# Optimization experiments

Hardware: AMD Instinct MI355X
Metric: run time of the kernel (lower is better)

Reference implementation:

```python
import jax, jax.numpy as jnp
import numpy as np

MAX_ITER = 10   # float32 branch of cg()
TOL = 1e-10

def _cdot(a, b):
    # complex_dot: sum(conj(a) * b) over all elements
    return jnp.sum(jnp.conj(a) * b)

def _A(p, smaps, mask):
    # p: [H,W] complex, smaps: [C,H,W] complex, mask: [H,W] real
    return jnp.fft.fft2(smaps * p[None], norm='ortho') * mask[None]

def _AH(y, smaps, mask):
    imgs = jnp.fft.ifft2(y * mask[None], norm='ortho')
    return jnp.sum(jnp.conj(smaps) * imgs, axis=0)  # [H,W]

def _cg(M, rhs):
    # conjugate gradient, faithful to the TF while_loop body
    def cond(s):
        i, rTr, x, r, p = s
        return jnp.logical_and(i < MAX_ITER, rTr > TOL)
    def body(s):
        i, rTr, x, r, p = s
        Ap = M(p)
        alpha = rTr / jnp.real(_cdot(p, Ap))
        x = x + p * alpha
        r = r - Ap * alpha
        rTrNew = jnp.real(_cdot(r, r))
        beta = rTrNew / rTr
        p = r + p * beta
        return (i + 1, rTrNew, x, r, p)
    rTr0 = jnp.real(_cdot(rhs, rhs))
    s0 = (jnp.int32(0), rTr0, jnp.zeros_like(rhs), rhs, rhs)
    return jax.lax.while_loop(cond, body, s0)[2]

def _solve_one(lambdaa, rhs, smaps, mask):
    M = lambda p: _AH(_A(p, smaps, mask), smaps, mask) + p * lambdaa
    return _cg(M, rhs)

_solve_b = jax.vmap(_solve_one, in_axes=(None, 0, 0, 0))  # replaces map_fn
_AH_b = jax.vmap(_AH, in_axes=(0, 0, 0))

def setup_inputs():
    key = jax.random.key(0)
    ks = jax.random.split(key, 7)
    B, C, H, W = 4, 16, 384, 384
    f = lambda k, s: jax.random.normal(k, s, dtype=jnp.float32)
    return {
        'lambdaa': 0.05 * jnp.ones((), jnp.float32),
        'x_re': f(ks[0], (B, H, W)),
        'x_im': f(ks[1], (B, H, W)),
        'y_re': f(ks[2], (B, C, H, W)),
        'y_im': f(ks[3], (B, C, H, W)),
        'smaps_re': f(ks[4], (B, C, H, W)),
        'smaps_im': f(ks[5], (B, C, H, W)),
        'mask': (jax.random.uniform(ks[6], (B, H, W)) < 0.33).astype(jnp.float32),
    }

def reference(lambdaa, x_re, x_im, y_re, y_im, smaps_re, smaps_im, mask):
    x = jax.lax.complex(x_re, x_im)
    y = jax.lax.complex(y_re, y_im)
    smaps = jax.lax.complex(smaps_re, smaps_im)
    # rhs = AH(y) + lambdaa * x
    rhs = _AH_b(y, smaps, mask) + x * lambdaa
    out = _solve_b(lambdaa, rhs, smaps, mask)  # [B,H,W] complex
    return jnp.stack([out.real, out.imag], axis=-1)  # [B,H,W,2] float32
```

## Files before the change

### kernel.cpp

```cpp
#include <hip/hip_runtime.h>
#include <hip/hip_fp16.h>


#define Bn 4
#define Cn 16
#define Hn 384
#define Wn 384
#define NPIX (Hn*Wn)
#define NPIX2 (NPIX/2)
#define TPB 256
#define CTPB 512
#define NCOL 16
#define TOLF 1e-10f
#define NITER 10
#define RED_BLKS 72
#define GRP 4
#define CPG 4
#define RPITCH 416
#define CPITCH 417

__device__ __forceinline__ float2 cadd(float2 a, float2 b){ return make_float2(a.x+b.x, a.y+b.y); }
__device__ __forceinline__ float2 csub(float2 a, float2 b){ return make_float2(a.x-b.x, a.y-b.y); }
__device__ __forceinline__ float2 cmulf(float2 a, float2 b){
  return make_float2(a.x*b.x - a.y*b.y, a.x*b.y + a.y*b.x);
}

__device__ __forceinline__ void wave_fence(){ asm volatile("s_waitcnt lgkmcnt(0)" ::: "memory"); }

template<int IMM>
__device__ __forceinline__ float2 shx(float2 v){
  int x = __builtin_amdgcn_ds_swizzle(__float_as_int(v.x), IMM);
  int y = __builtin_amdgcn_ds_swizzle(__float_as_int(v.y), IMM);
  return make_float2(__int_as_float(x), __int_as_float(y));
}

__device__ __forceinline__ int rev5(int x){
  return ((x&1)<<4) | ((x&2)<<2) | (x&4) | ((x&8)>>2) | ((x&16)>>4);
}

__device__ __forceinline__ int offmap(int w){ return w + ((w*683)>>13); }

template<int DIR>
__device__ __forceinline__ void fft12(float2* v)
{
  const float S3 = (DIR<0) ? -0.86602540378443864676f : 0.86602540378443864676f;
  const float sg = (DIR<0) ? -1.f : 1.f;
  float2 t[4][3];
#pragma unroll
  for (int b = 0; b < 4; ++b) {
    float2 a0 = v[b], a1 = v[4+b], a2 = v[8+b];
    float2 s = cadd(a1,a2), d = csub(a1,a2);
    float2 mm = make_float2(a0.x - 0.5f*s.x, a0.y - 0.5f*s.y);
    float2 e  = make_float2(-d.y*S3, d.x*S3);
    t[b][0] = cadd(a0,s);
    t[b][1] = cadd(mm,e);
    t[b][2] = csub(mm,e);
  }
  const float2 w1  = make_float2(0.86602540378443864676f, sg*0.5f);
  const float2 w2  = make_float2(0.5f, sg*0.86602540378443864676f);
  const float2 w3  = make_float2(0.f, sg);
  const float2 w4t = make_float2(-0.5f, sg*0.86602540378443864676f);
  const float2 w6  = make_float2(-1.f, 0.f);
  t[1][1] = cmulf(t[1][1], w1);  t[1][2] = cmulf(t[1][2], w2);
  t[2][1] = cmulf(t[2][1], w2);  t[2][2] = cmulf(t[2][2], w4t);
  t[3][1] = cmulf(t[3][1], w3);  t[3][2] = cmulf(t[3][2], w6);
#pragma unroll
  for (int c = 0; c < 3; ++c) {
    float2 e = cadd(t[0][c], t[2][c]);
    float2 f = csub(t[0][c], t[2][c]);
    float2 g = cadd(t[1][c], t[3][c]);
    float2 h = csub(t[1][c], t[3][c]);
    float2 ih = (DIR<0) ? make_float2(h.y, -h.x) : make_float2(-h.y, h.x);
    v[c]   = cadd(e,g);
    v[c+3] = cadd(f,ih);
    v[c+6] = csub(e,g);
    v[c+9] = csub(f,ih);
  }
}

template<int DIR>
__device__ __forceinline__ void fft32_lanes(float2* v, int li)
{
  const float c2pi = (DIR<0) ? -6.2831853071795864769f : 6.2831853071795864769f;
  const float sg   = (DIR<0) ? -1.f : 1.f;
  float s, c;
  __sincosf(c2pi*(1.f/32.f)*(float)(li&15), &s, &c); float2 wA = make_float2(c,s);
  __sincosf(c2pi*(1.f/16.f)*(float)(li&7),  &s, &c); float2 wB = make_float2(c,s);
  __sincosf(c2pi*(1.f/ 8.f)*(float)(li&3),  &s, &c); float2 wC = make_float2(c,s);
  bool bA = li & 16, bB = li & 8, bC = li & 4, bD = li & 2, bE = li & 1;
#pragma unroll
  for (int k = 0; k < 12; ++k) {
    float2 a = v[k], o;
    o = shx<0x401F>(a); a = bA ? cmulf(csub(o,a), wA) : cadd(a,o);
    o = shx<0x201F>(a); a = bB ? cmulf(csub(o,a), wB) : cadd(a,o);
    o = shx<0x101F>(a); a = bC ? cmulf(csub(o,a), wC) : cadd(a,o);
    o = shx<0x081F>(a);
    { float2 su = cadd(a,o), d = csub(o,a);
      float2 dw = bE ? make_float2(-sg*d.y, sg*d.x) : d;
      a = bD ? dw : su; }
    o = shx<0x041F>(a); a = bE ? csub(o,a) : cadd(a,o);
    v[k] = a;
  }
}

template<int DIR>
__device__ __forceinline__ void fft32_lanes_dit(float2* v, int li)
{
  const float c2pi = (DIR<0) ? -6.2831853071795864769f : 6.2831853071795864769f;
  const float sg   = (DIR<0) ? -1.f : 1.f;
  float s, c;
  __sincosf(c2pi*(1.f/32.f)*(float)(li&15), &s, &c); float2 wA = make_float2(c,s);
  __sincosf(c2pi*(1.f/16.f)*(float)(li&7),  &s, &c); float2 wB = make_float2(c,s);
  __sincosf(c2pi*(1.f/ 8.f)*(float)(li&3),  &s, &c); float2 wC = make_float2(c,s);
  bool bA = li & 16, bB = li & 8, bC = li & 4, bD = li & 2, bE = li & 1;
#pragma unroll
  for (int k = 0; k < 12; ++k) {
    float2 a = v[k], o;
    o = shx<0x041F>(a); a = bE ? csub(o,a) : cadd(a,o);
    { float2 aw = make_float2(-sg*a.y, sg*a.x);
      a = (bD && bE) ? aw : a;
      o = shx<0x081F>(a); a = bD ? csub(o,a) : cadd(a,o); }
    { float2 aw = cmulf(a, wC); a = bC ? aw : a;
      o = shx<0x101F>(a); a = bC ? csub(o,a) : cadd(a,o); }
    { float2 aw = cmulf(a, wB); a = bB ? aw : a;
      o = shx<0x201F>(a); a = bB ? csub(o,a) : cadd(a,o); }
    { float2 aw = cmulf(a, wA); a = bA ? aw : a;
      o = shx<0x401F>(a); a = bA ? csub(o,a) : cadd(a,o); }
    v[k] = a;
  }
}

template<int DIR>
__device__ __forceinline__ void fft384(float2* v, int li)
{
  fft12<DIR>(v);
  const float c2pi = (DIR<0) ? -6.2831853071795864769f : 6.2831853071795864769f;
  float s, c;
  __sincosf(c2pi*(1.f/384.f)*(float)li, &s, &c);
  float2 W = make_float2(c,s), cw = W;
#pragma unroll
  for (int k = 1; k < 12; ++k) { v[k] = cmulf(v[k], cw); cw = cmulf(cw, W); }
  fft32_lanes<DIR>(v, li);
}

template<int DIR>
__device__ __forceinline__ void fft384_scr(float2* v, int li)
{
  fft32_lanes_dit<DIR>(v, li);
  const float c2pi = (DIR<0) ? -6.2831853071795864769f : 6.2831853071795864769f;
  float s, c;
  __sincosf(c2pi*(1.f/384.f)*(float)li, &s, &c);
  float2 W = make_float2(c,s), cw = W;
#pragma unroll
  for (int k = 1; k < 12; ++k) { v[k] = cmulf(v[k], cw); cw = cmulf(cw, W); }
  fft12<DIR>(v);
}


template<bool HS>
__global__ __launch_bounds__(TPB) void k_row_fwd(
    const float2* __restrict__ p, const float* __restrict__ Sre,
    const float* __restrict__ Sim, const __half2* __restrict__ Sh,
    __half2* __restrict__ tmp)
{
  int tid = threadIdx.x;
  int wave = tid>>6, lane = tid&63, sub = lane>>5, li = lane&31;
  int row = wave*2 + sub;
  int tile = blockIdx.x % (Hn/8);
  int bc   = blockIdx.x / (Hn/8);
  int b = bc / Cn;
  int h = tile*8 + row;
  size_t gbase = (size_t)bc*NPIX + (size_t)h*Wn;
  size_t pbase = (size_t)b*NPIX + (size_t)h*Wn;

  float2 v[12];
#pragma unroll
  for (int k = 0; k < 12; ++k) {
    int w = 32*k + li;
    float2 pv = p[pbase + w];
    float sr, si;
    if (HS) { float2 sv = __half22float2(Sh[gbase + w]); sr = sv.x; si = sv.y; }
    else    { sr = Sre[gbase + w]; si = Sim[gbase + w]; }
    v[k] = make_float2(sr*pv.x - si*pv.y, sr*pv.y + si*pv.x);
  }
  fft384<-1>(v, li);
#pragma unroll
  for (int k = 0; k < 12; ++k)
    tmp[gbase + 32*k + li] = __float22half2_rn(v[k]);
}

template<bool HS>
__global__ __launch_bounds__(TPB) void k_row_inv_scr(
    const __half2* __restrict__ tmp, const float* __restrict__ Sre,
    const float* __restrict__ Sim, const __half2* __restrict__ Sh,
    float2* __restrict__ partial)
{
  int tid = threadIdx.x;
  int wave = tid>>6, lane = tid&63, sub = lane>>5, li = lane&31;
  int row = wave*2 + sub;
  int tile = blockIdx.x % (Hn/8);
  int rest = blockIdx.x / (Hn/8);
  int g = rest % GRP;
  int b = rest / GRP;
  int h = tile*8 + row;

  size_t gbase0 = ((size_t)b*Cn + g*CPG)*NPIX + (size_t)h*Wn;
  __half2 hb[12];
#pragma unroll
  for (int k = 0; k < 12; ++k) hb[k] = tmp[gbase0 + 32*k + li];

  float2 acc[12];
#pragma unroll
  for (int k = 0; k < 12; ++k) acc[k] = make_float2(0.f, 0.f);

  for (int j = 0; j < CPG; ++j) {
    size_t gb = gbase0 + (size_t)j*NPIX;
    float2 vc[12];
#pragma unroll
    for (int k = 0; k < 12; ++k) vc[k] = __half22float2(hb[k]);
    if (j + 1 < CPG) {
      size_t gbn = gb + NPIX;
#pragma unroll
      for (int k = 0; k < 12; ++k) hb[k] = tmp[gbn + 32*k + li];
    }
    fft384_scr<1>(vc, li);
#pragma unroll
    for (int k = 0; k < 12; ++k) {
      int w = 32*k + li;
      float sr, si;
      if (HS) { float2 sv = __half22float2(Sh[gb + w]); sr = sv.x; si = sv.y; }
      else    { sr = Sre[gb + w]; si = Sim[gb + w]; }
      acc[k].x += sr*vc[k].x + si*vc[k].y;
      acc[k].y += sr*vc[k].y - si*vc[k].x;
    }
  }
  size_t pbase = ((size_t)g*Bn + b)*NPIX + (size_t)h*Wn;
#pragma unroll
  for (int k = 0; k < 12; ++k) partial[pbase + 32*k + li] = acc[k];
}

__global__ __launch_bounds__(TPB) void k_row_inv_nat(
    const __half2* __restrict__ tmp, const float* __restrict__ Sre,
    const float* __restrict__ Sim, float2* __restrict__ partial)
{
  __shared__ float2 lbuf[8*RPITCH];
  int tid = threadIdx.x;
  int wave = tid>>6, lane = tid&63, sub = lane>>5, li = lane&31;
  int row = wave*2 + sub;
  int tile = blockIdx.x % (Hn/8);
  int rest = blockIdx.x / (Hn/8);
  int g = rest % GRP;
  int b = rest / GRP;
  int h = tile*8 + row;
  int m = rev5(li);
  float2* lrow = lbuf + row*RPITCH;

  size_t gbase0 = ((size_t)b*Cn + g*CPG)*NPIX + (size_t)h*Wn;
  __half2 hb[12];
#pragma unroll
  for (int k = 0; k < 12; ++k) hb[k] = tmp[gbase0 + 32*k + li];

  float2 acc[12];
#pragma unroll
  for (int k = 0; k < 12; ++k) acc[k] = make_float2(0.f, 0.f);

  for (int j = 0; j < CPG; ++j) {
    size_t gb = gbase0 + (size_t)j*NPIX;
    float2 vc[12];
#pragma unroll
    for (int k = 0; k < 12; ++k) vc[k] = __half22float2(hb[k]);
    if (j + 1 < CPG) {
      size_t gbn = gb + NPIX;
#pragma unroll
      for (int k = 0; k < 12; ++k) hb[k] = tmp[gbn + 32*k + li];
    }
    fft384<1>(vc, li);
    wave_fence();
#pragma unroll
    for (int k = 0; k < 12; ++k) lrow[13*m + k] = vc[k];
    wave_fence();
#pragma unroll
    for (int k = 0; k < 12; ++k) {
      int w = 32*k + li;
      float2 u = lrow[offmap(w)];
      float sr = Sre[gb + w], si = Sim[gb + w];
      acc[k].x += sr*u.x + si*u.y;
      acc[k].y += sr*u.y - si*u.x;
    }
  }
  size_t pbase = ((size_t)g*Bn + b)*NPIX + (size_t)h*Wn;
#pragma unroll
  for (int k = 0; k < 12; ++k) partial[pbase + 32*k + li] = acc[k];
}

__global__ __launch_bounds__(TPB) void k_spack(
    const float* __restrict__ sre, const float* __restrict__ sim,
    __half2* __restrict__ sh)
{
  size_t i = (size_t)blockIdx.x*TPB + threadIdx.x;
  if (i < (size_t)Bn*Cn*NPIX) sh[i] = __floats2half2_rn(sre[i], sim[i]);
}

__global__ __launch_bounds__(TPB) void k_maskp(
    const float* __restrict__ mask, float* __restrict__ maskP,
    float* __restrict__ scal)
{
  int idx = blockIdx.x*TPB + threadIdx.x;
  if (blockIdx.x == 0) scal[threadIdx.x] = 0.0f;
  if (idx >= Bn*NPIX) return;
  int k = idx % 12; int t = idx / 12;
  int li = t & 31; t >>= 5;
  int wa = t % Wn; int b = t / Wn;
  int wt = (wa >> 5) + 12*rev5(wa & 31);
  maskP[idx] = mask[((size_t)b*Hn + (k + 12*rev5(li)))*Wn + wt] * (1.0f/(float)NPIX);
}

__global__ __launch_bounds__(CTPB) void k_col_full(
    __half2* __restrict__ tmp, const float* __restrict__ maskP)
{
  __shared__ __half2 dbuf[NCOL*CPITCH];
  int tid = threadIdx.x;
  int wave = tid>>6, lane = tid&63, sub = lane>>5, li = lane&31;
  int col = wave*2 + sub;
  int tile = blockIdx.x % (Wn/NCOL);
  int bc   = blockIdx.x / (Wn/NCOL);
  int b = bc / Cn;
  int w0 = tile*NCOL;
  size_t tbase = (size_t)bc*NPIX;

  for (int e = tid; e < NCOL*Hn; e += CTPB) {
    int wi = e & (NCOL-1), h = e >> 4;
    dbuf[wi*CPITCH + offmap(h)] = tmp[tbase + (size_t)h*Wn + w0 + wi];
  }
  __syncthreads();

  __half2* drow = dbuf + col*CPITCH;
  int w = w0 + col;
  const float4* mp4 = (const float4*)(maskP + (((size_t)b*Wn + w)*32 + li)*12);
  float4 m0 = mp4[0], m1 = mp4[1], m2 = mp4[2];
  float2 v[12];
#pragma unroll
  for (int k = 0; k < 12; ++k) v[k] = __half22float2(drow[offmap(32*k + li)]);
  fft384<-1>(v, li);
  float mk[12] = {m0.x,m0.y,m0.z,m0.w, m1.x,m1.y,m1.z,m1.w, m2.x,m2.y,m2.z,m2.w};
#pragma unroll
  for (int k = 0; k < 12; ++k) v[k] = make_float2(v[k].x*mk[k], v[k].y*mk[k]);
  fft384_scr<1>(v, li);
#pragma unroll
  for (int k = 0; k < 12; ++k) drow[offmap(32*k + li)] = __float22half2_rn(v[k]);
  __syncthreads();

  for (int e = tid; e < NCOL*Hn; e += CTPB) {
    int wi = e & (NCOL-1), h = e >> 4;
    tmp[tbase + (size_t)h*Wn + w0 + wi] = dbuf[wi*CPITCH + offmap(h)];
  }
}

__global__ __launch_bounds__(CTPB) void k_col_rhs(
    const float* __restrict__ yre, const float* __restrict__ yim,
    const float* __restrict__ mask, __half2* __restrict__ tmp)
{
  __shared__ float2 dbuf[NCOL*CPITCH];
  int tid = threadIdx.x;
  int wave = tid>>6, lane = tid&63, sub = lane>>5, li = lane&31;
  int col = wave*2 + sub;
  int tile = blockIdx.x % (Wn/NCOL);
  int bc   = blockIdx.x / (Wn/NCOL);
  int b = bc / Cn;
  int w0 = tile*NCOL;
  size_t tbase = (size_t)bc*NPIX;
  size_t mbase = (size_t)b*NPIX;

  for (int e = tid; e < NCOL*Hn; e += CTPB) {
    int wi = e & (NCOL-1), h = e >> 4;
    size_t gi = (size_t)h*Wn + w0 + wi;
    float mv = mask[mbase + gi] * (1.0f/384.0f);
    dbuf[wi*CPITCH + offmap(h)] = make_float2(yre[tbase+gi]*mv, yim[tbase+gi]*mv);
  }
  __syncthreads();

  float2* drow = dbuf + col*CPITCH;
  int m = rev5(li);
  float2 v[12];
#pragma unroll
  for (int k = 0; k < 12; ++k) v[k] = drow[offmap(32*k + li)];
  fft384<1>(v, li);
  wave_fence();
#pragma unroll
  for (int k = 0; k < 12; ++k) drow[13*m + k] = v[k];
  __syncthreads();

  for (int e = tid; e < NCOL*Hn; e += CTPB) {
    int wi = e & (NCOL-1), h = e >> 4;
    tmp[tbase + (size_t)h*Wn + w0 + wi] = __float22half2_rn(dbuf[wi*CPITCH + offmap(h)]);
  }
}


__device__ __forceinline__ void block_reduce_atomic(float sum, float* target)
{
  __shared__ float red[TPB];
  red[threadIdx.x] = sum; __syncthreads();
  for (int s = TPB/2; s > 0; s >>= 1) {
    if (threadIdx.x < s) red[threadIdx.x] += red[threadIdx.x + s];
    __syncthreads();
  }
  if (threadIdx.x == 0) unsafeAtomicAdd(target, red[0]);
  __syncthreads();
}

__global__ __launch_bounds__(TPB) void k_rhs_init(
    const float* __restrict__ xre, const float* __restrict__ xim,
    const float* __restrict__ lam, const float2* __restrict__ partial,
    float2* __restrict__ r, float2* __restrict__ p, float2* __restrict__ x,
    float* __restrict__ scal)
{
  int b = blockIdx.y;
  float l = lam[0];
  float sum = 0.0f;
  const float2* xr2 = (const float2*)(xre + (size_t)b*NPIX);
  const float2* xi2 = (const float2*)(xim + (size_t)b*NPIX);
  float4* r4 = (float4*)(r + (size_t)b*NPIX);
  float4* p4 = (float4*)(p + (size_t)b*NPIX);
  float4* x4 = (float4*)(x + (size_t)b*NPIX);
  for (int i = blockIdx.x*TPB + threadIdx.x; i < NPIX2; i += RED_BLKS*TPB) {
    float2 re = xr2[i], im = xi2[i];
    float4 rv = make_float4(l*re.x, l*im.x, l*re.y, l*im.y);
#pragma unroll
    for (int g = 0; g < GRP; ++g) {
      float4 pv = ((const float4*)(partial + ((size_t)g*Bn + b)*NPIX))[i];
      rv.x += pv.x; rv.y += pv.y; rv.z += pv.z; rv.w += pv.w;
    }
    r4[i] = rv; p4[i] = rv;
    x4[i] = make_float4(0.f, 0.f, 0.f, 0.f);
    sum += rv.x*rv.x + rv.y*rv.y + rv.z*rv.z + rv.w*rv.w;
  }
  block_reduce_atomic(sum, &scal[b]);
}

__global__ __launch_bounds__(TPB) void k_combine_dot3(
    const float2* __restrict__ p, const float2* __restrict__ r,
    const float* __restrict__ lam, const float2* __restrict__ partial,
    float2* __restrict__ Ap, float* __restrict__ slot)
{
  int b = blockIdx.y;
  float l = lam[0];
  float s_pAp = 0.f, s_AA = 0.f, s_rA = 0.f;
  const float4* p4 = (const float4*)(p + (size_t)b*NPIX);
  const float4* r4 = (const float4*)(r + (size_t)b*NPIX);
  float4* A4 = (float4*)(Ap + (size_t)b*NPIX);
  for (int i = blockIdx.x*TPB + threadIdx.x; i < NPIX2; i += RED_BLKS*TPB) {
    float4 pv = p4[i];
    float4 av = make_float4(l*pv.x, l*pv.y, l*pv.z, l*pv.w);
#pragma unroll
    for (int g = 0; g < GRP; ++g) {
      float4 qv = ((const float4*)(partial + ((size_t)g*Bn + b)*NPIX))[i];
      av.x += qv.x; av.y += qv.y; av.z += qv.z; av.w += qv.w;
    }
    A4[i] = av;
    float4 rv = r4[i];
    s_pAp += pv.x*av.x + pv.y*av.y + pv.z*av.z + pv.w*av.w;
    s_AA  += av.x*av.x + av.y*av.y + av.z*av.z + av.w*av.w;
    s_rA  += rv.x*av.x + rv.y*av.y + rv.z*av.z + rv.w*av.w;
  }
  block_reduce_atomic(s_pAp, &slot[b]);
  block_reduce_atomic(s_AA,  &slot[4+b]);
  block_reduce_atomic(s_rA,  &slot[8+b]);
}

__global__ void k_scal(float* __restrict__ scal, int it)
{
  int b = threadIdx.x;
  if (b >= Bn) return;
  float rtr = scal[it*4 + b];
  const float* slot = scal + 64 + it*12;
  float* ab = scal + 224 + it*12;
  bool act = rtr > TOLF;
  float alpha = act ? rtr / slot[b] : 0.f;
  float rtrn = act ? fmaxf(rtr - 2.f*alpha*slot[8+b] + alpha*alpha*slot[4+b], 0.f) : rtr;
  float beta = act ? rtrn / rtr : 0.f;
  scal[(it+1)*4 + b] = rtrn;
  ab[b] = alpha; ab[4+b] = beta; ab[8+b] = act ? 1.f : 0.f;
}

__global__ __launch_bounds__(TPB) void k_upd(
    float2* __restrict__ x, float2* __restrict__ r, float2* __restrict__ p,
    const float2* __restrict__ Ap, const float* __restrict__ ab)
{
  int b = blockIdx.y;
  if (!(ab[8+b] > 0.5f)) return;
  float alpha = ab[b], beta = ab[4+b];
  float4* x4 = (float4*)(x + (size_t)b*NPIX);
  float4* r4 = (float4*)(r + (size_t)b*NPIX);
  float4* p4 = (float4*)(p + (size_t)b*NPIX);
  const float4* A4 = (const float4*)(Ap + (size_t)b*NPIX);
  for (int i = blockIdx.x*TPB + threadIdx.x; i < NPIX2; i += RED_BLKS*TPB) {
    float4 pv = p4[i], av = A4[i], xv = x4[i], rv = r4[i];
    xv.x += alpha*pv.x; xv.y += alpha*pv.y; xv.z += alpha*pv.z; xv.w += alpha*pv.w;
    rv.x -= alpha*av.x; rv.y -= alpha*av.y; rv.z -= alpha*av.z; rv.w -= alpha*av.w;
    x4[i] = xv; r4[i] = rv;
    p4[i] = make_float4(rv.x + beta*pv.x, rv.y + beta*pv.y,
                        rv.z + beta*pv.z, rv.w + beta*pv.w);
  }
}


extern "C" void kernel_launch(void* const* d_in, const int* in_sizes, int n_in,
                              void* d_out, int out_size, void* d_ws, size_t ws_size,
                              hipStream_t stream)
{
  const float* lam  = (const float*)d_in[0];
  const float* xre  = (const float*)d_in[1];
  const float* xim  = (const float*)d_in[2];
  const float* yre  = (const float*)d_in[3];
  const float* yim  = (const float*)d_in[4];
  const float* sre  = (const float*)d_in[5];
  const float* sim  = (const float*)d_in[6];
  const float* mask = (const float*)d_in[7];

  const size_t szTmp  = (size_t)Bn*Cn*NPIX*sizeof(__half2);
  const size_t szVec  = (size_t)Bn*NPIX*sizeof(float2);
  const size_t szMask = (size_t)Bn*NPIX*sizeof(float);
  const size_t szSh   = (size_t)Bn*Cn*NPIX*sizeof(__half2);
  const size_t base   = szTmp + (size_t)GRP*szVec + 3*szVec + 2048 + szMask;
  const bool useSh    = (ws_size >= base + szSh);

  char* ws = (char*)d_ws;
  __half2* tmp = (__half2*)ws;  ws += szTmp;
  float2* part = (float2*)ws;   ws += (size_t)GRP*szVec;
  float2* r    = (float2*)ws;   ws += szVec;
  float2* p    = (float2*)ws;   ws += szVec;
  float2* Ap   = (float2*)ws;   ws += szVec;
  float*  scal = (float*)ws;    ws += 2048;
  float*  mskP = (float*)ws;    ws += szMask;
  __half2* Sh  = (__half2*)ws;
  float2* x    = (float2*)d_out;

  dim3 blk(TPB);
  dim3 rg(RED_BLKS, Bn);
  int grid_row = Bn*Cn*(Hn/8);
  int grid_col = Bn*Cn*(Wn/NCOL);
  int grid_inv = Bn*GRP*(Hn/8);

  k_maskp<<<(Bn*NPIX)/TPB, blk, 0, stream>>>(mask, mskP, scal);
  if (useSh)
    k_spack<<<(Bn*Cn*NPIX)/TPB, blk, 0, stream>>>(sre, sim, Sh);

  k_col_rhs<<<grid_col, CTPB, 0, stream>>>(yre, yim, mask, tmp);
  k_row_inv_nat<<<grid_inv, blk, 0, stream>>>(tmp, sre, sim, part);
  k_rhs_init<<<rg, blk, 0, stream>>>(xre, xim, lam, part, r, p, x, scal);

  for (int it = 0; it < NITER; ++it) {
    if (useSh) {
      k_row_fwd<true><<<grid_row, blk, 0, stream>>>(p, sre, sim, Sh, tmp);
      k_col_full<<<grid_col, CTPB, 0, stream>>>(tmp, mskP);
      k_row_inv_scr<true><<<grid_inv, blk, 0, stream>>>(tmp, sre, sim, Sh, part);
    } else {
      k_row_fwd<false><<<grid_row, blk, 0, stream>>>(p, sre, sim, Sh, tmp);
      k_col_full<<<grid_col, CTPB, 0, stream>>>(tmp, mskP);
      k_row_inv_scr<false><<<grid_inv, blk, 0, stream>>>(tmp, sre, sim, Sh, part);
    }
    k_combine_dot3<<<rg, blk, 0, stream>>>(p, r, lam, part, Ap, scal + 64 + it*12);
    k_scal<<<1, 64, 0, stream>>>(scal, it);
    k_upd<<<rg, blk, 0, stream>>>(x, r, p, Ap, scal + 224 + it*12);
  }
}
```

Baseline: 1.454 ms.

## Use DPP lane exchanges in FFT butterflies and fold scalar update into k_upd

Most lane-exchange steps in the radix-2 FFT butterflies now use DPP moves instead of ds_swizzle, which avoids the LDS crossbar path and its lgkmcnt waits. The distance-16 exchange still uses swizzle, and the distance-4 exchange takes two DPP moves. Separately, the per-iteration k_scal launch is removed and each k_upd block recomputes alpha and beta from the reduction slots itself, with one thread writing the new residual norm. This drops ten tiny kernel launches at the cost of redundant scalar math per block. The DPP control codes must match the old swizzle lane pairings exactly, or the FFT results will be wrong.

```diff
diff --git a/kernel.cpp b/kernel.cpp
--- a/kernel.cpp
+++ b/kernel.cpp
@@ -34,6 +34,18 @@
   return make_float2(__int_as_float(x), __int_as_float(y));
 }
 
+template<int CTRL>
+__device__ __forceinline__ float2 dpp2(float2 v){
+  int x = __builtin_amdgcn_mov_dpp(__float_as_int(v.x), CTRL, 0xF, 0xF, true);
+  int y = __builtin_amdgcn_mov_dpp(__float_as_int(v.y), CTRL, 0xF, 0xF, true);
+  return make_float2(__int_as_float(x), __int_as_float(y));
+}
+__device__ __forceinline__ float2 xchg1 (float2 v){ return dpp2<0xB1>(v);  }
+__device__ __forceinline__ float2 xchg2 (float2 v){ return dpp2<0x4E>(v);  }
+__device__ __forceinline__ float2 xchg4 (float2 v){ return dpp2<0x1B>(dpp2<0x141>(v)); }
+__device__ __forceinline__ float2 xchg8 (float2 v){ return dpp2<0x128>(v); }
+__device__ __forceinline__ float2 xchg16(float2 v){ return shx<0x401F>(v); }
+
 __device__ __forceinline__ int rev5(int x){
   return ((x&1)<<4) | ((x&2)<<2) | (x&4) | ((x&8)>>2) | ((x&16)>>4);
 }
@@ -91,14 +103,14 @@
 #pragma unroll
   for (int k = 0; k < 12; ++k) {
     float2 a = v[k], o;
-    o = shx<0x401F>(a); a = bA ? cmulf(csub(o,a), wA) : cadd(a,o);
-    o = shx<0x201F>(a); a = bB ? cmulf(csub(o,a), wB) : cadd(a,o);
-    o = shx<0x101F>(a); a = bC ? cmulf(csub(o,a), wC) : cadd(a,o);
-    o = shx<0x081F>(a);
+    o = xchg16(a); a = bA ? cmulf(csub(o,a), wA) : cadd(a,o);
+    o = xchg8 (a); a = bB ? cmulf(csub(o,a), wB) : cadd(a,o);
+    o = xchg4 (a); a = bC ? cmulf(csub(o,a), wC) : cadd(a,o);
+    o = xchg2 (a);
     { float2 su = cadd(a,o), d = csub(o,a);
       float2 dw = bE ? make_float2(-sg*d.y, sg*d.x) : d;
       a = bD ? dw : su; }
-    o = shx<0x041F>(a); a = bE ? csub(o,a) : cadd(a,o);
+    o = xchg1 (a); a = bE ? csub(o,a) : cadd(a,o);
     v[k] = a;
   }
 }
@@ -116,16 +128,16 @@
 #pragma unroll
   for (int k = 0; k < 12; ++k) {
     float2 a = v[k], o;
-    o = shx<0x041F>(a); a = bE ? csub(o,a) : cadd(a,o);
+    o = xchg1(a); a = bE ? csub(o,a) : cadd(a,o);
     { float2 aw = make_float2(-sg*a.y, sg*a.x);
       a = (bD && bE) ? aw : a;
-      o = shx<0x081F>(a); a = bD ? csub(o,a) : cadd(a,o); }
+      o = xchg2(a); a = bD ? csub(o,a) : cadd(a,o); }
     { float2 aw = cmulf(a, wC); a = bC ? aw : a;
-      o = shx<0x101F>(a); a = bC ? csub(o,a) : cadd(a,o); }
+      o = xchg4(a); a = bC ? csub(o,a) : cadd(a,o); }
     { float2 aw = cmulf(a, wB); a = bB ? aw : a;
-      o = shx<0x201F>(a); a = bB ? csub(o,a) : cadd(a,o); }
+      o = xchg8(a); a = bB ? csub(o,a) : cadd(a,o); }
     { float2 aw = cmulf(a, wA); a = bA ? aw : a;
-      o = shx<0x401F>(a); a = bA ? csub(o,a) : cadd(a,o); }
+      o = xchg16(a); a = bA ? csub(o,a) : cadd(a,o); }
     v[k] = a;
   }
 }
@@ -468,28 +480,19 @@
   block_reduce_atomic(s_rA,  &slot[8+b]);
 }
 
-__global__ void k_scal(float* __restrict__ scal, int it)
-{
-  int b = threadIdx.x;
-  if (b >= Bn) return;
+__global__ __launch_bounds__(TPB) void k_upd(
+    float2* __restrict__ x, float2* __restrict__ r, float2* __restrict__ p,
+    const float2* __restrict__ Ap, float* __restrict__ scal, int it)
+{
+  int b = blockIdx.y;
   float rtr = scal[it*4 + b];
   const float* slot = scal + 64 + it*12;
-  float* ab = scal + 224 + it*12;
   bool act = rtr > TOLF;
   float alpha = act ? rtr / slot[b] : 0.f;
   float rtrn = act ? fmaxf(rtr - 2.f*alpha*slot[8+b] + alpha*alpha*slot[4+b], 0.f) : rtr;
   float beta = act ? rtrn / rtr : 0.f;
-  scal[(it+1)*4 + b] = rtrn;
-  ab[b] = alpha; ab[4+b] = beta; ab[8+b] = act ? 1.f : 0.f;
-}
-
-__global__ __launch_bounds__(TPB) void k_upd(
-    float2* __restrict__ x, float2* __restrict__ r, float2* __restrict__ p,
-    const float2* __restrict__ Ap, const float* __restrict__ ab)
-{
-  int b = blockIdx.y;
-  if (!(ab[8+b] > 0.5f)) return;
-  float alpha = ab[b], beta = ab[4+b];
+  if (blockIdx.x == 0 && threadIdx.x == 0) scal[(it+1)*4 + b] = rtrn;
+  if (!act) return;
   float4* x4 = (float4*)(x + (size_t)b*NPIX);
   float4* r4 = (float4*)(r + (size_t)b*NPIX);
   float4* p4 = (float4*)(p + (size_t)b*NPIX);
@@ -561,7 +564,6 @@
       k_row_inv_scr<false><<<grid_inv, blk, 0, stream>>>(tmp, sre, sim, Sh, part);
     }
     k_combine_dot3<<<rg, blk, 0, stream>>>(p, r, lam, part, Ap, scal + 64 + it*12);
-    k_scal<<<1, 64, 0, stream>>>(scal, it);
-    k_upd<<<rg, blk, 0, stream>>>(x, r, p, Ap, scal + 224 + it*12);
-  }
-}
+    k_upd<<<rg, blk, 0, stream>>>(x, r, p, Ap, scal, it);
+  }
+}
```

After: 1.393 ms. -4.2%, faster.
